# Performance work log

Measured on AMD Instinct MI355X. Metric: run time of the kernel, lower is better.

The kernel has to match this reference:

```python
import jax, jax.numpy as jnp
import numpy as np

N_NODES = 50000
N_EDGES = 800000
IN_DIM = 128
HIDDEN = 128
CLASSES = 64


def setup_inputs() -> dict:
    key = jax.random.key(0)
    ks = jax.random.split(key, 10)
    features = jax.random.normal(ks[0], (N_NODES, IN_DIM), dtype=jnp.float32)
    W1 = jax.random.normal(ks[1], (HIDDEN, IN_DIM), dtype=jnp.float32) * (2.0 / np.sqrt(IN_DIM + HIDDEN))
    b1 = jnp.zeros((HIDDEN,), dtype=jnp.float32)
    W2 = jax.random.normal(ks[2], (CLASSES, HIDDEN), dtype=jnp.float32) * (2.0 / np.sqrt(HIDDEN + CLASSES))
    b2 = jnp.zeros((CLASSES,), dtype=jnp.float32)
    order_attn = jax.random.uniform(ks[3], (2,), dtype=jnp.float32)
    src1 = jax.random.randint(ks[4], (N_EDGES,), 0, N_NODES, dtype=jnp.int32)
    dst1 = jax.random.randint(ks[5], (N_EDGES,), 0, N_NODES, dtype=jnp.int32)
    src2 = jax.random.randint(ks[6], (N_EDGES,), 0, N_NODES, dtype=jnp.int32)
    dst2 = jax.random.randint(ks[7], (N_EDGES,), 0, N_NODES, dtype=jnp.int32)
    return {"features": features, "W1": W1, "b1": b1, "W2": W2, "b2": b2,
            "order_attn": order_attn, "src1": src1, "dst1": dst1,
            "src2": src2, "dst2": dst2}


def _gin_conv(x, src, dst, W, b):
    # DGL GINConv, aggregator_type='sum', eps=0 (default, non-learnable):
    # h_v = Linear( x_v + sum_{(u->v) in E} x_u )
    agg = jax.ops.segment_sum(x[src], dst, num_segments=N_NODES)  # [N, D]
    return (x + agg) @ W.T + b


def reference(features, W1, b1, W2, b2, order_attn, src1, dst1, src2, dst2):
    a0, a1 = order_attn[0], order_attn[1]
    # layer 1 over both order-graphs
    x11 = jax.nn.elu(a0 * _gin_conv(features, src1, dst1, W1, b1))
    x12 = jax.nn.elu(a1 * _gin_conv(features, src2, dst2, W1, b1))
    x1 = x11 + x12  # [N, hidden]
    # layer 2 over both order-graphs
    x21 = jax.nn.elu(a0 * _gin_conv(x1, src1, dst1, W2, b2))
    x22 = jax.nn.elu(a1 * _gin_conv(x1, src2, dst2, W2, b2))
    return x21 + x22  # [N, classes]
```

## Files before the change

kernel.cpp:

```cpp
#include <hip/hip_runtime.h>
#include <math.h>

#define N_NODES 50000
#define N_EDGES 800000
#define IN_DIM 128
#define HIDDEN 128
#define CLASSES 64
#define N2 100000

#define BIN_SHIFT 9
#define NB 196
#define NBLK 192
#define CHUNK ((2 * N_EDGES + NBLK - 1) / NBLK)

static __device__ __forceinline__ float elu_f(float x) {
    return x > 0.f ? x : (expf(x) - 1.f);
}

static __device__ __forceinline__ void fma4(float4& a, const float4 w, const float s) {
    a.x = fmaf(w.x, s, a.x);
    a.y = fmaf(w.y, s, a.y);
    a.z = fmaf(w.z, s, a.z);
    a.w = fmaf(w.w, s, a.w);
}

static __device__ __forceinline__ unsigned pack_bf2(float a, float b) {
    unsigned ua = __float_as_uint(a);
    ua = (ua + 0x7FFFu + ((ua >> 16) & 1u)) >> 16;
    unsigned ub = __float_as_uint(b);
    ub = (ub + 0x7FFFu + ((ub >> 16) & 1u)) >> 16;
    return ua | (ub << 16);
}

static __device__ __forceinline__ float2 bf2f2(unsigned u) {
    float2 r;
    r.x = __uint_as_float(u << 16);
    r.y = __uint_as_float(u & 0xFFFF0000u);
    return r;
}

__global__ __launch_bounds__(1024) void k_p1_count(
    const int* __restrict__ dst1, const int* __restrict__ dst2,
    int* __restrict__ counts)
{
    __shared__ int hist[NB];
    const int t = threadIdx.x, b = blockIdx.x;
    if (t < NB) hist[t] = 0;
    __syncthreads();
    const int beg = b * CHUNK;
    const int end = min(beg + CHUNK, 2 * N_EDGES);
    for (int i = beg + t; i < end; i += 1024) {
        const int idx = (i < N_EDGES) ? dst1[i] : (N_NODES + dst2[i - N_EDGES]);
        atomicAdd(&hist[idx >> BIN_SHIFT], 1);
    }
    __syncthreads();
    if (t < NB) counts[b * NB + t] = hist[t];
}

__global__ __launch_bounds__(256) void k_scan_bins(
    int* __restrict__ counts, int* __restrict__ binStart, int* __restrict__ off)
{
    __shared__ int tot[256];
    const int t = threadIdx.x;
    int total = 0;
    if (t < NB) {
        #pragma unroll 8
        for (int blk = 0; blk < NBLK; ++blk) total += counts[blk * NB + t];
    }
    tot[t] = (t < NB) ? total : 0;
    __syncthreads();
    const int v = tot[t];
    for (int d = 1; d < 256; d <<= 1) {
        const int x = (t >= d) ? tot[t - d] : 0;
        __syncthreads();
        tot[t] += x;
        __syncthreads();
    }
    const int excl = tot[t] - v;
    if (t < NB) binStart[t] = excl;
    if (t == NB - 1) binStart[NB] = tot[t];
    if (t == 0) off[N2] = 2 * N_EDGES;
    if (t < NB) {
        int run = excl;
        #pragma unroll 8
        for (int blk = 0; blk < NBLK; ++blk) {
            const int c = counts[blk * NB + t];
            counts[blk * NB + t] = run;
            run += c;
        }
    }
}

__global__ __launch_bounds__(1024) void k_p2_scatter(
    const int* __restrict__ src1, const int* __restrict__ dst1,
    const int* __restrict__ src2, const int* __restrict__ dst2,
    const int* __restrict__ counts, unsigned* __restrict__ binned)
{
    __shared__ int cur[NB];
    const int t = threadIdx.x, b = blockIdx.x;
    if (t < NB) cur[t] = counts[b * NB + t];
    __syncthreads();
    const int beg = b * CHUNK;
    const int end = min(beg + CHUNK, 2 * N_EDGES);
    for (int i = beg + t; i < end; i += 1024) {
        int s, idx;
        if (i < N_EDGES) { s = src1[i]; idx = dst1[i]; }
        else             { s = src2[i - N_EDGES]; idx = N_NODES + dst2[i - N_EDGES]; }
        const int bin = idx >> BIN_SHIFT;
        const unsigned rec = ((unsigned)s << BIN_SHIFT) | (unsigned)(idx & 511);
        const int pos = atomicAdd(&cur[bin], 1);
        binned[pos] = rec;
    }
}

__global__ __launch_bounds__(1024) void k_p3_csr(
    const unsigned* __restrict__ binned, const int* __restrict__ binStart,
    int* __restrict__ off, int* __restrict__ csr)
{
    __shared__ int hist[512], sc[512], cur[512];
    const int t = threadIdx.x, bin = blockIdx.x;
    const int bs = binStart[bin], be = binStart[bin + 1];
    const int base = bin << BIN_SHIFT;
    const int nloc = min(512, N2 - base);
    if (t < 512) hist[t] = 0;
    __syncthreads();
    for (int p = bs + t; p < be; p += 1024)
        atomicAdd(&hist[binned[p] & 511u], 1);
    __syncthreads();
    int v = 0;
    if (t < 512) { v = hist[t]; sc[t] = v; }
    __syncthreads();
    for (int d = 1; d < 512; d <<= 1) {
        int x = 0;
        if (t < 512 && t >= d) x = sc[t - d];
        __syncthreads();
        if (t < 512) sc[t] += x;
        __syncthreads();
    }
    if (t < 512) {
        const int excl = sc[t] - v;
        cur[t] = bs + excl;
        if (t < nloc) off[base + t] = bs + excl;
    }
    __syncthreads();
    for (int p = bs + t; p < be; p += 1024) {
        const unsigned rec = binned[p];
        const int pos = atomicAdd(&cur[rec & 511u], 1);
        csr[pos] = (int)(rec >> BIN_SHIFT);
    }
}

__global__ __launch_bounds__(256) void k_gemm1(
    const float* __restrict__ f, const float* __restrict__ W1,
    unsigned short* __restrict__ y1b)
{
    __shared__ float Wt[IN_DIM][HIDDEN + 4];
    __shared__ float S[16][IN_DIM];

    const int t = threadIdx.x;
    for (int i = t; i < HIDDEN * IN_DIM; i += 256) {
        const int o = i >> 7, k = i & 127;
        Wt[k][o] = W1[i];
    }
    const int o4 = (t & 31) * 4;
    const int ln = t >> 5;

    const int ntiles = N_NODES / 16;
    for (int tile = blockIdx.x; tile < ntiles; tile += gridDim.x) {
        const int v0 = tile * 16;
        __syncthreads();
        for (int i = t; i < 16 * IN_DIM; i += 256) {
            const int r = i >> 7, k = i & 127;
            S[r][k] = f[(size_t)(v0 + r) * IN_DIM + k];
        }
        __syncthreads();

        float4 acc1 = {0.f, 0.f, 0.f, 0.f};
        float4 acc2 = {0.f, 0.f, 0.f, 0.f};
        const float* s1 = S[ln * 2];
        const float* s2 = S[ln * 2 + 1];
        #pragma unroll 8
        for (int k = 0; k < IN_DIM; k += 4) {
            const float4 sa = *reinterpret_cast<const float4*>(s1 + k);
            const float4 sb = *reinterpret_cast<const float4*>(s2 + k);
            const float4 w0 = *reinterpret_cast<const float4*>(&Wt[k + 0][o4]);
            const float4 w1 = *reinterpret_cast<const float4*>(&Wt[k + 1][o4]);
            const float4 w2 = *reinterpret_cast<const float4*>(&Wt[k + 2][o4]);
            const float4 w3 = *reinterpret_cast<const float4*>(&Wt[k + 3][o4]);
            fma4(acc1, w0, sa.x); fma4(acc1, w1, sa.y); fma4(acc1, w2, sa.z); fma4(acc1, w3, sa.w);
            fma4(acc2, w0, sb.x); fma4(acc2, w1, sb.y); fma4(acc2, w2, sb.z); fma4(acc2, w3, sb.w);
        }
        const int na = v0 + ln * 2, nb = na + 1;
        uint2 pa, pb;
        pa.x = pack_bf2(acc1.x, acc1.y); pa.y = pack_bf2(acc1.z, acc1.w);
        pb.x = pack_bf2(acc2.x, acc2.y); pb.y = pack_bf2(acc2.z, acc2.w);
        *reinterpret_cast<uint2*>(y1b + (size_t)na * HIDDEN + o4) = pa;
        *reinterpret_cast<uint2*>(y1b + (size_t)nb * HIDDEN + o4) = pb;
    }
}

__global__ __launch_bounds__(256) void k_gemm2(
    const float* __restrict__ x1, const float* __restrict__ W2,
    unsigned short* __restrict__ y2b)
{
    __shared__ float Wt[IN_DIM][CLASSES + 4];
    __shared__ float S[32][IN_DIM];

    const int t = threadIdx.x;
    for (int i = t; i < CLASSES * IN_DIM; i += 256) {
        const int c = i >> 7, k = i & 127;
        Wt[k][c] = W2[i];
    }
    const int c4 = (t & 15) * 4;
    const int ln = t >> 4;

    const int ntiles = (N_NODES + 31) / 32;
    for (int tile = blockIdx.x; tile < ntiles; tile += gridDim.x) {
        const int v0 = tile * 32;
        __syncthreads();
        for (int i = t; i < 32 * IN_DIM; i += 256) {
            const int r = i >> 7, k = i & 127;
            const int node = v0 + r;
            S[r][k] = (node < N_NODES) ? x1[(size_t)node * IN_DIM + k] : 0.f;
        }
        __syncthreads();

        float4 acc1 = {0.f, 0.f, 0.f, 0.f};
        float4 acc2 = {0.f, 0.f, 0.f, 0.f};
        const float* s1 = S[ln * 2];
        const float* s2 = S[ln * 2 + 1];
        #pragma unroll 8
        for (int k = 0; k < IN_DIM; k += 4) {
            const float4 sa = *reinterpret_cast<const float4*>(s1 + k);
            const float4 sb = *reinterpret_cast<const float4*>(s2 + k);
            const float4 w0 = *reinterpret_cast<const float4*>(&Wt[k + 0][c4]);
            const float4 w1 = *reinterpret_cast<const float4*>(&Wt[k + 1][c4]);
            const float4 w2 = *reinterpret_cast<const float4*>(&Wt[k + 2][c4]);
            const float4 w3 = *reinterpret_cast<const float4*>(&Wt[k + 3][c4]);
            fma4(acc1, w0, sa.x); fma4(acc1, w1, sa.y); fma4(acc1, w2, sa.z); fma4(acc1, w3, sa.w);
            fma4(acc2, w0, sb.x); fma4(acc2, w1, sb.y); fma4(acc2, w2, sb.z); fma4(acc2, w3, sb.w);
        }
        const int na = v0 + ln * 2, nb = na + 1;
        uint2 pa, pb;
        pa.x = pack_bf2(acc1.x, acc1.y); pa.y = pack_bf2(acc1.z, acc1.w);
        pb.x = pack_bf2(acc2.x, acc2.y); pb.y = pack_bf2(acc2.z, acc2.w);
        if (na < N_NODES) *reinterpret_cast<uint2*>(y2b + (size_t)na * CLASSES + c4) = pa;
        if (nb < N_NODES) *reinterpret_cast<uint2*>(y2b + (size_t)nb * CLASSES + c4) = pb;
    }
}

__global__ __launch_bounds__(256) void k_pull1(
    const unsigned short* __restrict__ y1b,
    const int* __restrict__ off, const int* __restrict__ csr,
    const float* __restrict__ b1, const float* __restrict__ attn,
    float* __restrict__ x1)
{
    const int lane = threadIdx.x & 63;
    const int v = (blockIdx.x * 256 + threadIdx.x) >> 6;
    if (v >= N_NODES) return;
    const int c = lane * 2;

    float2 acc1 = {0.f, 0.f}, acc2 = {0.f, 0.f};
    #pragma unroll
    for (int g = 0; g < 2; ++g) {
        const int idx = g * N_NODES + v;
        const int beg = off[idx], end_ = off[idx + 1];
        float2 acc = {0.f, 0.f};
        int j = beg;
        for (; j + 4 <= end_; j += 4) {
            const int s0 = csr[j], s1 = csr[j + 1], s2 = csr[j + 2], s3 = csr[j + 3];
            const float2 r0 = bf2f2(*reinterpret_cast<const unsigned*>(y1b + (size_t)s0 * HIDDEN + c));
            const float2 r1 = bf2f2(*reinterpret_cast<const unsigned*>(y1b + (size_t)s1 * HIDDEN + c));
            const float2 r2 = bf2f2(*reinterpret_cast<const unsigned*>(y1b + (size_t)s2 * HIDDEN + c));
            const float2 r3 = bf2f2(*reinterpret_cast<const unsigned*>(y1b + (size_t)s3 * HIDDEN + c));
            acc.x += (r0.x + r1.x) + (r2.x + r3.x);
            acc.y += (r0.y + r1.y) + (r2.y + r3.y);
        }
        for (; j < end_; ++j) {
            const int s = csr[j];
            const float2 r = bf2f2(*reinterpret_cast<const unsigned*>(y1b + (size_t)s * HIDDEN + c));
            acc.x += r.x; acc.y += r.y;
        }
        if (g == 0) acc1 = acc; else acc2 = acc;
    }

    const float2 yv = bf2f2(*reinterpret_cast<const unsigned*>(y1b + (size_t)v * HIDDEN + c));
    const float2 bb = *reinterpret_cast<const float2*>(b1 + c);
    const float a0 = attn[0], a1 = attn[1];
    float2 r;
    r.x = elu_f(a0 * (yv.x + acc1.x + bb.x)) + elu_f(a1 * (yv.x + acc2.x + bb.x));
    r.y = elu_f(a0 * (yv.y + acc1.y + bb.y)) + elu_f(a1 * (yv.y + acc2.y + bb.y));
    *reinterpret_cast<float2*>(x1 + (size_t)v * HIDDEN + c) = r;
}

__global__ __launch_bounds__(256) void k_pull2(
    const unsigned short* __restrict__ y2b,
    const int* __restrict__ off, const int* __restrict__ csr,
    const float* __restrict__ b2, const float* __restrict__ attn,
    float* __restrict__ out)
{
    const int lane = threadIdx.x & 63;
    const int v = (blockIdx.x * 256 + threadIdx.x) >> 6;
    if (v >= N_NODES) return;
    const int half = lane >> 5;
    const int l = lane & 31;
    const int c = l * 2;

    const int idx = half * N_NODES + v;
    const int beg = off[idx], end_ = off[idx + 1];
    float2 acc = {0.f, 0.f};
    int j = beg;
    for (; j + 4 <= end_; j += 4) {
        const int s0 = csr[j], s1 = csr[j + 1], s2 = csr[j + 2], s3 = csr[j + 3];
        const float2 r0 = bf2f2(*reinterpret_cast<const unsigned*>(y2b + (size_t)s0 * CLASSES + c));
        const float2 r1 = bf2f2(*reinterpret_cast<const unsigned*>(y2b + (size_t)s1 * CLASSES + c));
        const float2 r2 = bf2f2(*reinterpret_cast<const unsigned*>(y2b + (size_t)s2 * CLASSES + c));
        const float2 r3 = bf2f2(*reinterpret_cast<const unsigned*>(y2b + (size_t)s3 * CLASSES + c));
        acc.x += (r0.x + r1.x) + (r2.x + r3.x);
        acc.y += (r0.y + r1.y) + (r2.y + r3.y);
    }
    for (; j < end_; ++j) {
        const int s = csr[j];
        const float2 r = bf2f2(*reinterpret_cast<const unsigned*>(y2b + (size_t)s * CLASSES + c));
        acc.x += r.x; acc.y += r.y;
    }

    float2 other;
    other.x = __shfl(acc.x, lane ^ 32);
    other.y = __shfl(acc.y, lane ^ 32);
    const float2 g1 = (half == 0) ? acc : other;
    const float2 g2 = (half == 0) ? other : acc;

    const float2 yv = bf2f2(*reinterpret_cast<const unsigned*>(y2b + (size_t)v * CLASSES + c));
    const float2 bb = *reinterpret_cast<const float2*>(b2 + c);
    const float a0 = attn[0], a1 = attn[1];
    float2 r;
    r.x = elu_f(a0 * (yv.x + g1.x + bb.x)) + elu_f(a1 * (yv.x + g2.x + bb.x));
    r.y = elu_f(a0 * (yv.y + g1.y + bb.y)) + elu_f(a1 * (yv.y + g2.y + bb.y));
    if (half == 0)
        *reinterpret_cast<float2*>(out + (size_t)v * CLASSES + c) = r;
}

extern "C" void kernel_launch(void* const* d_in, const int* in_sizes, int n_in,
                              void* d_out, int out_size, void* d_ws, size_t ws_size,
                              hipStream_t stream)
{
    const float* features = (const float*)d_in[0];
    const float* W1   = (const float*)d_in[1];
    const float* b1   = (const float*)d_in[2];
    const float* W2   = (const float*)d_in[3];
    const float* b2   = (const float*)d_in[4];
    const float* attn = (const float*)d_in[5];
    const int* src1   = (const int*)d_in[6];
    const int* dst1   = (const int*)d_in[7];
    const int* src2   = (const int*)d_in[8];
    const int* dst2   = (const int*)d_in[9];
    float* out = (float*)d_out;

    float* x1 = (float*)d_ws;
    unsigned short* y1b = (unsigned short*)(x1 + (size_t)N_NODES * HIDDEN);
    unsigned short* y2b = y1b + (size_t)N_NODES * HIDDEN;
    int* off      = (int*)(y2b + (size_t)N_NODES * CLASSES);
    int* binStart = off + (N2 + 1);
    int* counts   = binStart + (NB + 1);
    unsigned* binned = (unsigned*)(counts + NBLK * NB);
    int* csr      = (int*)(binned + 2 * N_EDGES);

    k_p1_count  <<<NBLK, 1024, 0, stream>>>(dst1, dst2, counts);
    k_scan_bins <<<1, 256, 0, stream>>>(counts, binStart, off);
    k_p2_scatter<<<NBLK, 1024, 0, stream>>>(src1, dst1, src2, dst2, counts, binned);
    k_p3_csr    <<<NB, 1024, 0, stream>>>(binned, binStart, off, csr);

    k_gemm1<<<3125, 256, 0, stream>>>(features, W1, y1b);
    k_pull1<<<12500, 256, 0, stream>>>(y1b, off, csr, b1, attn, x1);

    k_gemm2<<<1563, 256, 0, stream>>>(x1, W2, y2b);
    k_pull2<<<12500, 256, 0, stream>>>(y2b, off, csr, b2, attn, out);
}
```

Measured before the change: 325.1 us.

## Use finer CSR bins, transposed counts, masked 8-way gather unroll, fewer GEMM blocks

Halves the CSR bin size to 256 nodes, giving 391 bins, and raises the histogram block count to 256. The per-block counts are stored bin-major so the scan kernel can read and write them as int4 vectors. Both pull kernels replace the unroll-by-4-plus-remainder loop with an always-8-wide masked gather, clamping the index and multiplying by zero, to put more loads in flight per wave at the cost of some wasted loads on the tail. The GEMM launches use fewer blocks, which is only correct if those kernels loop over rows with a grid stride.

Result: no change. 329.8 us (+1.5%).

```diff
diff --git a/kernel.cpp b/kernel.cpp
--- a/kernel.cpp
+++ b/kernel.cpp
@@ -8,9 +8,10 @@
 #define CLASSES 64
 #define N2 100000
 
-#define BIN_SHIFT 9
-#define NB 196
-#define NBLK 192
+#define BIN_SHIFT 8
+#define BIN_SZ 256
+#define NB 391
+#define NBLK 256
 #define CHUNK ((2 * N_EDGES + NBLK - 1) / NBLK)
 
 static __device__ __forceinline__ float elu_f(float x) {
@@ -54,23 +55,27 @@
         atomicAdd(&hist[idx >> BIN_SHIFT], 1);
     }
     __syncthreads();
-    if (t < NB) counts[b * NB + t] = hist[t];
-}
-
-__global__ __launch_bounds__(256) void k_scan_bins(
+    if (t < NB) counts[t * NBLK + b] = hist[t];
+}
+
+__global__ __launch_bounds__(512) void k_scan_bins(
     int* __restrict__ counts, int* __restrict__ binStart, int* __restrict__ off)
 {
-    __shared__ int tot[256];
+    __shared__ int tot[512];
     const int t = threadIdx.x;
     int total = 0;
     if (t < NB) {
+        const int4* p = reinterpret_cast<const int4*>(counts + t * NBLK);
         #pragma unroll 8
-        for (int blk = 0; blk < NBLK; ++blk) total += counts[blk * NB + t];
+        for (int i = 0; i < NBLK / 4; ++i) {
+            const int4 c = p[i];
+            total += (c.x + c.y) + (c.z + c.w);
+        }
     }
     tot[t] = (t < NB) ? total : 0;
     __syncthreads();
     const int v = tot[t];
-    for (int d = 1; d < 256; d <<= 1) {
+    for (int d = 1; d < 512; d <<= 1) {
         const int x = (t >= d) ? tot[t - d] : 0;
         __syncthreads();
         tot[t] += x;
@@ -82,11 +87,15 @@
     if (t == 0) off[N2] = 2 * N_EDGES;
     if (t < NB) {
         int run = excl;
-        #pragma unroll 8
-        for (int blk = 0; blk < NBLK; ++blk) {
-            const int c = counts[blk * NB + t];
-            counts[blk * NB + t] = run;
-            run += c;
+        int* p = counts + t * NBLK;
+        for (int i = 0; i < NBLK; i += 4) {
+            int4 c = *reinterpret_cast<int4*>(p + i);
+            int4 w;
+            w.x = run; run += c.x;
+            w.y = run; run += c.y;
+            w.z = run; run += c.z;
+            w.w = run; run += c.w;
+            *reinterpret_cast<int4*>(p + i) = w;
         }
     }
 }
@@ -98,7 +107,7 @@
 {
     __shared__ int cur[NB];
     const int t = threadIdx.x, b = blockIdx.x;
-    if (t < NB) cur[t] = counts[b * NB + t];
+    if (t < NB) cur[t] = counts[t * NBLK + b];
     __syncthreads();
     const int beg = b * CHUNK;
     const int end = min(beg + CHUNK, 2 * N_EDGES);
@@ -107,7 +116,7 @@
         if (i < N_EDGES) { s = src1[i]; idx = dst1[i]; }
         else             { s = src2[i - N_EDGES]; idx = N_NODES + dst2[i - N_EDGES]; }
         const int bin = idx >> BIN_SHIFT;
-        const unsigned rec = ((unsigned)s << BIN_SHIFT) | (unsigned)(idx & 511);
+        const unsigned rec = ((unsigned)s << BIN_SHIFT) | (unsigned)(idx & (BIN_SZ - 1));
         const int pos = atomicAdd(&cur[bin], 1);
         binned[pos] = rec;
     }
@@ -117,27 +126,27 @@
     const unsigned* __restrict__ binned, const int* __restrict__ binStart,
     int* __restrict__ off, int* __restrict__ csr)
 {
-    __shared__ int hist[512], sc[512], cur[512];
+    __shared__ int hist[BIN_SZ], sc[BIN_SZ], cur[BIN_SZ];
     const int t = threadIdx.x, bin = blockIdx.x;
     const int bs = binStart[bin], be = binStart[bin + 1];
     const int base = bin << BIN_SHIFT;
-    const int nloc = min(512, N2 - base);
-    if (t < 512) hist[t] = 0;
+    const int nloc = min(BIN_SZ, N2 - base);
+    if (t < BIN_SZ) hist[t] = 0;
     __syncthreads();
     for (int p = bs + t; p < be; p += 1024)
-        atomicAdd(&hist[binned[p] & 511u], 1);
+        atomicAdd(&hist[binned[p] & (BIN_SZ - 1u)], 1);
     __syncthreads();
     int v = 0;
-    if (t < 512) { v = hist[t]; sc[t] = v; }
-    __syncthreads();
-    for (int d = 1; d < 512; d <<= 1) {
+    if (t < BIN_SZ) { v = hist[t]; sc[t] = v; }
+    __syncthreads();
+    for (int d = 1; d < BIN_SZ; d <<= 1) {
         int x = 0;
-        if (t < 512 && t >= d) x = sc[t - d];
-        __syncthreads();
-        if (t < 512) sc[t] += x;
-        __syncthreads();
-    }
-    if (t < 512) {
+        if (t < BIN_SZ && t >= d) x = sc[t - d];
+        __syncthreads();
+        if (t < BIN_SZ) sc[t] += x;
+        __syncthreads();
+    }
+    if (t < BIN_SZ) {
         const int excl = sc[t] - v;
         cur[t] = bs + excl;
         if (t < nloc) off[base + t] = bs + excl;
@@ -145,7 +154,7 @@
     __syncthreads();
     for (int p = bs + t; p < be; p += 1024) {
         const unsigned rec = binned[p];
-        const int pos = atomicAdd(&cur[rec & 511u], 1);
+        const int pos = atomicAdd(&cur[rec & (BIN_SZ - 1u)], 1);
         csr[pos] = (int)(rec >> BIN_SHIFT);
     }
 }
@@ -266,20 +275,17 @@
         const int idx = g * N_NODES + v;
         const int beg = off[idx], end_ = off[idx + 1];
         float2 acc = {0.f, 0.f};
-        int j = beg;
-        for (; j + 4 <= end_; j += 4) {
-            const int s0 = csr[j], s1 = csr[j + 1], s2 = csr[j + 2], s3 = csr[j + 3];
-            const float2 r0 = bf2f2(*reinterpret_cast<const unsigned*>(y1b + (size_t)s0 * HIDDEN + c));
-            const float2 r1 = bf2f2(*reinterpret_cast<const unsigned*>(y1b + (size_t)s1 * HIDDEN + c));
-            const float2 r2 = bf2f2(*reinterpret_cast<const unsigned*>(y1b + (size_t)s2 * HIDDEN + c));
-            const float2 r3 = bf2f2(*reinterpret_cast<const unsigned*>(y1b + (size_t)s3 * HIDDEN + c));
-            acc.x += (r0.x + r1.x) + (r2.x + r3.x);
-            acc.y += (r0.y + r1.y) + (r2.y + r3.y);
-        }
-        for (; j < end_; ++j) {
-            const int s = csr[j];
-            const float2 r = bf2f2(*reinterpret_cast<const unsigned*>(y1b + (size_t)s * HIDDEN + c));
-            acc.x += r.x; acc.y += r.y;
+        for (int j = beg; j < end_; j += 8) {
+            #pragma unroll
+            for (int u = 0; u < 8; ++u) {
+                const int jj = j + u;
+                const int s = csr[min(jj, end_ - 1)];
+                const float2 r = bf2f2(*reinterpret_cast<const unsigned*>(
+                    y1b + (size_t)s * HIDDEN + c));
+                const float m = (jj < end_) ? 1.f : 0.f;
+                acc.x = fmaf(m, r.x, acc.x);
+                acc.y = fmaf(m, r.y, acc.y);
+            }
         }
         if (g == 0) acc1 = acc; else acc2 = acc;
     }
@@ -309,20 +315,17 @@
     const int idx = half * N_NODES + v;
     const int beg = off[idx], end_ = off[idx + 1];
     float2 acc = {0.f, 0.f};
-    int j = beg;
-    for (; j + 4 <= end_; j += 4) {
-        const int s0 = csr[j], s1 = csr[j + 1], s2 = csr[j + 2], s3 = csr[j + 3];
-        const float2 r0 = bf2f2(*reinterpret_cast<const unsigned*>(y2b + (size_t)s0 * CLASSES + c));
-        const float2 r1 = bf2f2(*reinterpret_cast<const unsigned*>(y2b + (size_t)s1 * CLASSES + c));
-        const float2 r2 = bf2f2(*reinterpret_cast<const unsigned*>(y2b + (size_t)s2 * CLASSES + c));
-        const float2 r3 = bf2f2(*reinterpret_cast<const unsigned*>(y2b + (size_t)s3 * CLASSES + c));
-        acc.x += (r0.x + r1.x) + (r2.x + r3.x);
-        acc.y += (r0.y + r1.y) + (r2.y + r3.y);
-    }
-    for (; j < end_; ++j) {
-        const int s = csr[j];
-        const float2 r = bf2f2(*reinterpret_cast<const unsigned*>(y2b + (size_t)s * CLASSES + c));
-        acc.x += r.x; acc.y += r.y;
+    for (int j = beg; j < end_; j += 8) {
+        #pragma unroll
+        for (int u = 0; u < 8; ++u) {
+            const int jj = j + u;
+            const int s = csr[min(jj, end_ - 1)];
+            const float2 r = bf2f2(*reinterpret_cast<const unsigned*>(
+                y2b + (size_t)s * CLASSES + c));
+            const float m = (jj < end_) ? 1.f : 0.f;
+            acc.x = fmaf(m, r.x, acc.x);
+            acc.y = fmaf(m, r.y, acc.y);
+        }
     }
 
     float2 other;
@@ -361,19 +364,19 @@
     unsigned short* y1b = (unsigned short*)(x1 + (size_t)N_NODES * HIDDEN);
     unsigned short* y2b = y1b + (size_t)N_NODES * HIDDEN;
     int* off      = (int*)(y2b + (size_t)N_NODES * CLASSES);
-    int* binStart = off + (N2 + 1);
-    int* counts   = binStart + (NB + 1);
-    unsigned* binned = (unsigned*)(counts + NBLK * NB);
+    int* binStart = off + (N2 + 4);
+    int* counts   = binStart + 392;
+    unsigned* binned = (unsigned*)(counts + NB * NBLK);
     int* csr      = (int*)(binned + 2 * N_EDGES);
 
     k_p1_count  <<<NBLK, 1024, 0, stream>>>(dst1, dst2, counts);
-    k_scan_bins <<<1, 256, 0, stream>>>(counts, binStart, off);
+    k_scan_bins <<<1, 512, 0, stream>>>(counts, binStart, off);
     k_p2_scatter<<<NBLK, 1024, 0, stream>>>(src1, dst1, src2, dst2, counts, binned);
     k_p3_csr    <<<NB, 1024, 0, stream>>>(binned, binStart, off, csr);
 
-    k_gemm1<<<3125, 256, 0, stream>>>(features, W1, y1b);
+    k_gemm1<<<1024, 256, 0, stream>>>(features, W1, y1b);
     k_pull1<<<12500, 256, 0, stream>>>(y1b, off, csr, b1, attn, x1);
 
-    k_gemm2<<<1563, 256, 0, stream>>>(x1, W2, y2b);
+    k_gemm2<<<782, 256, 0, stream>>>(x1, W2, y2b);
     k_pull2<<<12500, 256, 0, stream>>>(y2b, off, csr, b2, attn, out);
 }
```
